# Optimization experiments

Measured on AMD Instinct MI355X. Metric: run time of the kernel, lower is better.

Reference implementation:

```python
import jax, jax.numpy as jnp
import numpy as np

BETA = 0.25
EPS = 1e-12  # matches torch F.normalize default eps


def l2norm(x):
    # x / max(||x||_2, eps) over last dim, like torch.nn.functional.normalize
    n = jnp.linalg.norm(x, axis=-1, keepdims=True)
    return x / jnp.maximum(n, EPS)


def setup_inputs() -> dict:
    key = jax.random.key(0)
    kz, kw = jax.random.split(key)
    B, C, H, W = 16, 128, 32, 32
    K, D = 8192, 128
    z = jax.random.normal(kz, (B, C, H, W), dtype=jnp.float32)
    # kmeans_init=False path: randn then l2norm
    weight = l2norm(jax.random.normal(kw, (K, D), dtype=jnp.float32))
    return {"z": z, "weight": weight}


def reference(z, weight):
    B, C, H, W = z.shape
    # b c h w -> b h w c, then l2norm over channel dim
    zt = l2norm(jnp.transpose(z, (0, 2, 3, 1)))
    z_flat = zt.reshape(-1, C)                        # (N, D)
    x_sq = jnp.sum(z_flat * z_flat, axis=1, keepdims=True)      # (N, 1)
    c_sq = jnp.sum(weight * weight, axis=1)[None, :]            # (1, K)
    xc = jnp.einsum('nd,kd->nk', z_flat, weight)                # (N, K) GEMM
    dists = x_sq + c_sq - 2.0 * xc
    encoding_indices = jnp.argmin(dists, axis=1)                # (N,)
    z_q = weight[encoding_indices].reshape(zt.shape)            # (B,H,W,C)
    # commitment loss: beta * mse(stop_grad(z_q), z)
    loss = BETA * jnp.mean((jax.lax.stop_gradient(z_q) - zt) ** 2)
    # straight-through estimator
    z_q = zt + jax.lax.stop_gradient(z_q - zt)
    z_q = jnp.transpose(z_q, (0, 3, 1, 2))                      # b h w c -> b c h w
    return z_q, loss, encoding_indices
```

## Files before the change

kernel.cpp:

```cpp
#include <hip/hip_runtime.h>
#include <hip/hip_bf16.h>

typedef unsigned int u32;
typedef unsigned long long u64;
typedef unsigned short u16;

#define NPOS 16384
#define DCH  128
#define KCB  8192
#define HW   1024
#define BETA 0.25f
#define ZQ_SZ 2097152
#define MARGIN 0.022f
#define QCAP 8192
#define ZSTR 132

typedef __attribute__((ext_vector_type(8))) short short8;
typedef __attribute__((ext_vector_type(4))) float f32x4;

__device__ inline u16 f2bf(float x) {
    u32 u = __float_as_uint(x);
    return (u16)((u + 0x7FFFu + ((u >> 16) & 1u)) >> 16);
}
__device__ inline u32 mono(float f) {
    u32 b = __float_as_uint(f);
    return (b & 0x80000000u) ? ~b : (b | 0x80000000u);
}

__global__ __launch_bounds__(256) void kwprep(const float* __restrict__ w,
                                              u16* __restrict__ wb,
                                              float* __restrict__ csq) {
    const int t = threadIdx.x;
    const int row = blockIdx.x * 16 + (t >> 4);
    const int l = t & 15;
    const float4* src = (const float4*)(w + (size_t)row * DCH + l * 8);
    float4 a = src[0], b = src[1];
    float s = a.x*a.x + a.y*a.y + a.z*a.z + a.w*a.w
            + b.x*b.x + b.y*b.y + b.z*b.z + b.w*b.w;
    union { u16 h[8]; uint4 v; } u;
    u.h[0]=f2bf(a.x); u.h[1]=f2bf(a.y); u.h[2]=f2bf(a.z); u.h[3]=f2bf(a.w);
    u.h[4]=f2bf(b.x); u.h[5]=f2bf(b.y); u.h[6]=f2bf(b.z); u.h[7]=f2bf(b.w);
    *(uint4*)(wb + (size_t)row * DCH + l * 8) = u.v;
    s += __shfl_xor(s, 1, 64);
    s += __shfl_xor(s, 2, 64);
    s += __shfl_xor(s, 4, 64);
    s += __shfl_xor(s, 8, 64);
    if (l == 0) csq[row] = s;
}

__global__ __launch_bounds__(256, 2) void kmain(const float* __restrict__ z,
                                                const float* __restrict__ wgt,
                                                const u16* __restrict__ wb,
                                                const float* __restrict__ csq,
                                                float* __restrict__ out) {
    __shared__ __align__(16) float ztl[64 * ZSTR];
    __shared__ __align__(16) u32 shpool[64 * ZSTR];
    __shared__ u32 rowMinU[64];
    __shared__ u64 finalkey[64];
    __shared__ float psum[64][4];
    __shared__ float invL[64];
    __shared__ int codes[64];
    __shared__ float lsum[4];
    __shared__ int qcnt;

    const int t = threadIdx.x;
    const int lane = t & 63;
    const int w = t >> 6;
    const int n0 = blockIdx.x * 64;
    const int b = n0 >> 10, hw0 = n0 & 1023;

    const int p = lane;
    float vch[32];
    {
        const float* zp = z + (size_t)b * DCH * HW + hw0 + p;
        #pragma unroll
        for (int j = 0; j < 32; ++j)
            vch[j] = zp[(size_t)(w * 32 + j) * HW];
        float s = 0.f;
        #pragma unroll
        for (int j = 0; j < 32; ++j) s += vch[j] * vch[j];
        psum[p][w] = s;
    }
    if (t < 64) { rowMinU[t] = 0x7f800000u; finalkey[t] = ~0ULL; }
    if (t == 0) qcnt = 0;
    __syncthreads();
    if (t < 64) {
        float ss = psum[t][0] + psum[t][1] + psum[t][2] + psum[t][3];
        invL[t] = 1.0f / fmaxf(sqrtf(ss), 1e-12f);
    }
    __syncthreads();
    {
        float inv = invL[p];
        #pragma unroll
        for (int j = 0; j < 32; ++j)
            ztl[p * ZSTR + w * 32 + j] = vch[j] * inv;
    }
    __syncthreads();

    short8 af[4][4];
    #pragma unroll
    for (int rt = 0; rt < 4; ++rt)
        #pragma unroll
        for (int ks = 0; ks < 4; ++ks) {
            int row = rt * 16 + (lane & 15);
            int kb = ks * 32 + (lane >> 4) * 8;
            const float4* zr = (const float4*)&ztl[row * ZSTR + kb];
            float4 x0 = zr[0], x1 = zr[1];
            union { u16 h[8]; short8 v; } uu;
            uu.h[0]=f2bf(x0.x); uu.h[1]=f2bf(x0.y); uu.h[2]=f2bf(x0.z); uu.h[3]=f2bf(x0.w);
            uu.h[4]=f2bf(x1.x); uu.h[5]=f2bf(x1.y); uu.h[6]=f2bf(x1.z); uu.h[7]=f2bf(x1.w);
            af[rt][ks] = uu.v;
        }

    const u16* wtb = wb + ((w * 32 + (lane & 15)) << 7) + ((lane >> 4) << 3);

    float bmin[16], thr[16];
    #pragma unroll
    for (int i = 0; i < 16; ++i) { bmin[i] = 3.4e38f; thr[i] = -1.f; }

    short8 bA[8], bB[8];

#define LOADB(D, KT) do { \
    const u16* bsrc = wtb + (size_t)(KT) * 16384; \
    _Pragma("unroll") \
    for (int ct_ = 0; ct_ < 2; ++ct_) \
        _Pragma("unroll") \
        for (int ks_ = 0; ks_ < 4; ++ks_) \
            D[ct_ * 4 + ks_] = *(const short8*)(bsrc + ct_ * 2048 + ks_ * 32); \
} while (0)

#define COMPUTE(S, KT, COLLECT) do { \
    f32x4 acc[4][2] = {}; \
    _Pragma("unroll") \
    for (int ks_ = 0; ks_ < 4; ++ks_) \
        _Pragma("unroll") \
        for (int rt_ = 0; rt_ < 4; ++rt_) { \
            acc[rt_][0] = __builtin_amdgcn_mfma_f32_16x16x32_bf16(af[rt_][ks_], S[ks_],     acc[rt_][0], 0, 0, 0); \
            acc[rt_][1] = __builtin_amdgcn_mfma_f32_16x16x32_bf16(af[rt_][ks_], S[4 + ks_], acc[rt_][1], 0, 0, 0); \
        } \
    _Pragma("unroll") \
    for (int rt_ = 0; rt_ < 4; ++rt_) \
        _Pragma("unroll") \
        for (int e_ = 0; e_ < 4; ++e_) { \
            float d0 = fmaf(acc[rt_][0][e_], -2.f, 2.125f); \
            float d1 = fmaf(acc[rt_][1][e_], -2.f, 2.125f); \
            float m2 = fminf(d0, d1); \
            int i_ = rt_ * 4 + e_; \
            bmin[i_] = fminf(bmin[i_], m2); \
            if (COLLECT && m2 <= thr[i_]) { \
                u32 rl = (u32)(rt_ * 16 + (lane >> 4) * 4 + e_); \
                u32 cb = (u32)((KT) * 128 + w * 32 + (lane & 15)); \
                if (d0 <= thr[i_]) { int qi = atomicAdd(&qcnt, 1); if (qi < QCAP) shpool[qi] = (rl << 13) | cb; } \
                if (d1 <= thr[i_]) { int qi = atomicAdd(&qcnt, 1); if (qi < QCAP) shpool[qi] = (rl << 13) | (cb + 16u); } \
            } \
        } \
} while (0)

#define REFRESH() do { \
    _Pragma("unroll") \
    for (int i_ = 0; i_ < 16; ++i_) { \
        float v_ = bmin[i_]; \
        v_ = fminf(v_, __shfl_xor(v_, 1, 64)); \
        v_ = fminf(v_, __shfl_xor(v_, 2, 64)); \
        v_ = fminf(v_, __shfl_xor(v_, 4, 64)); \
        v_ = fminf(v_, __shfl_xor(v_, 8, 64)); \
        if ((lane & 15) == 0) \
            atomicMin(&rowMinU[(i_ >> 2) * 16 + (lane >> 4) * 4 + (i_ & 3)], __float_as_uint(v_)); \
    } \
    _Pragma("unroll") \
    for (int i_ = 0; i_ < 16; ++i_) \
        thr[i_] = fminf(__uint_as_float(rowMinU[(i_ >> 2) * 16 + (lane >> 4) * 4 + (i_ & 3)]), bmin[i_]) + MARGIN; \
} while (0)

    LOADB(bA, 0);
    COMPUTE(bA, 0, false);
    REFRESH();

    #pragma unroll 1
    for (int kt2 = 0; kt2 < 32; ++kt2) {
        const int kt0 = kt2 * 2;
        LOADB(bB, kt0 + 1);
        COMPUTE(bA, kt0, true);
        LOADB(bA, (kt0 + 2) & 63);
        COMPUTE(bB, kt0 + 1, true);
        if ((kt2 & 3) == 3) REFRESH();
    }

    __syncthreads();

    {
        int nq = qcnt < QCAP ? qcnt : QCAP;
        int gq = t >> 4, l = t & 15;
        for (int qi = gq; qi < nq; qi += 16) {
            u32 e = shpool[qi];
            int rl = e >> 13;
            int code = e & 0x1FFF;
            const float4* zr = (const float4*)&ztl[rl * ZSTR + l * 8];
            const float4* wr = (const float4*)(wgt + (size_t)code * DCH + l * 8);
            float4 za = zr[0], zb = zr[1], wa = wr[0], wbv = wr[1];
            float s = 0.f;
            s = fmaf(za.x, wa.x, s); s = fmaf(za.y, wa.y, s);
            s = fmaf(za.z, wa.z, s); s = fmaf(za.w, wa.w, s);
            s = fmaf(zb.x, wbv.x, s); s = fmaf(zb.y, wbv.y, s);
            s = fmaf(zb.z, wbv.z, s); s = fmaf(zb.w, wbv.w, s);
            s += __shfl_xor(s, 1, 64);
            s += __shfl_xor(s, 2, 64);
            s += __shfl_xor(s, 4, 64);
            s += __shfl_xor(s, 8, 64);
            if (l == 0) {
                float ed = csq[code] - 2.0f * s;
                u64 key = ((u64)mono(ed) << 32) | (u32)code;
                atomicMin((unsigned long long*)&finalkey[rl], (unsigned long long)key);
            }
        }
    }
    __syncthreads();

    if (t < 64) {
        u32 code = (u32)finalkey[t];
        codes[t] = (int)code;
        out[ZQ_SZ + 1 + n0 + t] = (float)code;
    }
    __syncthreads();
    float* Wg = (float*)shpool;
    {
        int r = t >> 2, c0 = (t & 3) * 32;
        const float4* wr = (const float4*)(wgt + (size_t)codes[r] * DCH + c0);
        float4* dst = (float4*)&Wg[r * ZSTR + c0];
        #pragma unroll
        for (int m = 0; m < 8; ++m) dst[m] = wr[m];
    }
    __syncthreads();
    {
        float* ob = out + (size_t)b * DCH * HW + hw0;
        float sq = 0.f;
        #pragma unroll
        for (int j = 0; j < 32; ++j) {
            int c = w * 32 + j;
            float zv = ztl[p * ZSTR + c];
            float diff = Wg[p * ZSTR + c] - zv;
            ob[(size_t)c * HW + p] = zv + diff;
            sq += diff * diff;
        }
        #pragma unroll
        for (int o = 32; o > 0; o >>= 1) sq += __shfl_down(sq, o, 64);
        if (lane == 0) lsum[w] = sq;
    }
    __syncthreads();
    if (t == 0)
        atomicAdd(out + ZQ_SZ, (lsum[0] + lsum[1] + lsum[2] + lsum[3]) * (BETA / (float)ZQ_SZ));

#undef LOADB
#undef COMPUTE
#undef REFRESH
}

extern "C" void kernel_launch(void* const* d_in, const int* in_sizes, int n_in,
                              void* d_out, int out_size, void* d_ws, size_t ws_size,
                              hipStream_t stream) {
    const float* z = (const float*)d_in[0];
    const float* w = (const float*)d_in[1];
    float* out = (float*)d_out;
    float* wsf = (float*)d_ws;

    u16* wb = (u16*)wsf;
    float* csq = wsf + 524288;

    kwprep<<<512, 256, 0, stream>>>(w, wb, csq);
    hipMemsetAsync(out + ZQ_SZ, 0, 4, stream);
    kmain<<<256, 256, 0, stream>>>(z, w, wb, csq, out);
}
```

Before: 200.2 us.

## Halve rows per block and double waves to fill all CUs

Each block now handles 32 positions with 512 threads instead of 64 positions with 256 threads, and the grid grows to 512 blocks. Each wave covers 16 codes per tile with two row tiles, and the candidate pool capacity shrinks. This is meant to use all compute units with more resident waves to hide load latency. In exchange, every block streams the full bf16 codebook for half as many rows, doubling codebook cache traffic and lowering MFMA work per load.

```diff
diff --git a/kernel.cpp b/kernel.cpp
--- a/kernel.cpp
+++ b/kernel.cpp
@@ -12,8 +12,9 @@
 #define BETA 0.25f
 #define ZQ_SZ 2097152
 #define MARGIN 0.022f
-#define QCAP 8192
+#define QCAP 2048
 #define ZSTR 132
+#define ROWS 32
 
 typedef __attribute__((ext_vector_type(8))) short short8;
 typedef __attribute__((ext_vector_type(4))) float f32x4;
@@ -48,58 +49,60 @@
     if (l == 0) csq[row] = s;
 }
 
-__global__ __launch_bounds__(256, 2) void kmain(const float* __restrict__ z,
+__global__ __launch_bounds__(512, 4) void kmain(const float* __restrict__ z,
                                                 const float* __restrict__ wgt,
                                                 const u16* __restrict__ wb,
                                                 const float* __restrict__ csq,
                                                 float* __restrict__ out) {
-    __shared__ __align__(16) float ztl[64 * ZSTR];
-    __shared__ __align__(16) u32 shpool[64 * ZSTR];
-    __shared__ u32 rowMinU[64];
-    __shared__ u64 finalkey[64];
-    __shared__ float psum[64][4];
-    __shared__ float invL[64];
-    __shared__ int codes[64];
-    __shared__ float lsum[4];
+    __shared__ __align__(16) float ztl[ROWS * ZSTR];
+    __shared__ __align__(16) u32 pool[ROWS * ZSTR];
+    __shared__ u32 rowMinU[ROWS];
+    __shared__ u64 finalkey[ROWS];
+    __shared__ float psum[ROWS][16];
+    __shared__ float invL[ROWS];
+    __shared__ int codes[ROWS];
+    __shared__ float lsum[8];
     __shared__ int qcnt;
 
     const int t = threadIdx.x;
     const int lane = t & 63;
     const int w = t >> 6;
-    const int n0 = blockIdx.x * 64;
+    const int n0 = blockIdx.x * ROWS;
     const int b = n0 >> 10, hw0 = n0 & 1023;
-
-    const int p = lane;
-    float vch[32];
+    const int p = t & 31, g = t >> 5;
+
+    float vch[8];
     {
         const float* zp = z + (size_t)b * DCH * HW + hw0 + p;
         #pragma unroll
-        for (int j = 0; j < 32; ++j)
-            vch[j] = zp[(size_t)(w * 32 + j) * HW];
+        for (int j = 0; j < 8; ++j)
+            vch[j] = zp[(size_t)(g + j * 16) * HW];
         float s = 0.f;
         #pragma unroll
-        for (int j = 0; j < 32; ++j) s += vch[j] * vch[j];
-        psum[p][w] = s;
-    }
-    if (t < 64) { rowMinU[t] = 0x7f800000u; finalkey[t] = ~0ULL; }
+        for (int j = 0; j < 8; ++j) s += vch[j] * vch[j];
+        psum[p][g] = s;
+    }
+    if (t < ROWS) { rowMinU[t] = 0x7f800000u; finalkey[t] = ~0ULL; }
     if (t == 0) qcnt = 0;
     __syncthreads();
-    if (t < 64) {
-        float ss = psum[t][0] + psum[t][1] + psum[t][2] + psum[t][3];
+    if (t < ROWS) {
+        float ss = 0.f;
+        #pragma unroll
+        for (int j = 0; j < 16; ++j) ss += psum[t][j];
         invL[t] = 1.0f / fmaxf(sqrtf(ss), 1e-12f);
     }
     __syncthreads();
     {
         float inv = invL[p];
         #pragma unroll
-        for (int j = 0; j < 32; ++j)
-            ztl[p * ZSTR + w * 32 + j] = vch[j] * inv;
-    }
-    __syncthreads();
-
-    short8 af[4][4];
+        for (int j = 0; j < 8; ++j)
+            ztl[p * ZSTR + g + j * 16] = vch[j] * inv;
+    }
+    __syncthreads();
+
+    short8 af[2][4];
     #pragma unroll
-    for (int rt = 0; rt < 4; ++rt)
+    for (int rt = 0; rt < 2; ++rt)
         #pragma unroll
         for (int ks = 0; ks < 4; ++ks) {
             int row = rt * 16 + (lane & 15);
@@ -112,53 +115,47 @@
             af[rt][ks] = uu.v;
         }
 
-    const u16* wtb = wb + ((w * 32 + (lane & 15)) << 7) + ((lane >> 4) << 3);
-
-    float bmin[16], thr[16];
+    const u16* wtb = wb + ((w * 16 + (lane & 15)) << 7) + ((lane >> 4) << 3);
+
+    float bmin[8], thr[8];
     #pragma unroll
-    for (int i = 0; i < 16; ++i) { bmin[i] = 3.4e38f; thr[i] = -1.f; }
-
-    short8 bA[8], bB[8];
+    for (int i = 0; i < 8; ++i) { bmin[i] = 3.4e38f; thr[i] = -1.f; }
+
+    short8 bA[4], bB[4];
 
 #define LOADB(D, KT) do { \
     const u16* bsrc = wtb + (size_t)(KT) * 16384; \
     _Pragma("unroll") \
-    for (int ct_ = 0; ct_ < 2; ++ct_) \
-        _Pragma("unroll") \
-        for (int ks_ = 0; ks_ < 4; ++ks_) \
-            D[ct_ * 4 + ks_] = *(const short8*)(bsrc + ct_ * 2048 + ks_ * 32); \
+    for (int ks_ = 0; ks_ < 4; ++ks_) \
+        D[ks_] = *(const short8*)(bsrc + ks_ * 32); \
 } while (0)
 
 #define COMPUTE(S, KT, COLLECT) do { \
-    f32x4 acc[4][2] = {}; \
-    _Pragma("unroll") \
-    for (int ks_ = 0; ks_ < 4; ++ks_) \
-        _Pragma("unroll") \
-        for (int rt_ = 0; rt_ < 4; ++rt_) { \
-            acc[rt_][0] = __builtin_amdgcn_mfma_f32_16x16x32_bf16(af[rt_][ks_], S[ks_],     acc[rt_][0], 0, 0, 0); \
-            acc[rt_][1] = __builtin_amdgcn_mfma_f32_16x16x32_bf16(af[rt_][ks_], S[4 + ks_], acc[rt_][1], 0, 0, 0); \
-        } \
-    _Pragma("unroll") \
-    for (int rt_ = 0; rt_ < 4; ++rt_) \
+    f32x4 acc[2] = {}; \
+    _Pragma("unroll") \
+    for (int ks_ = 0; ks_ < 4; ++ks_) { \
+        acc[0] = __builtin_amdgcn_mfma_f32_16x16x32_bf16(af[0][ks_], S[ks_], acc[0], 0, 0, 0); \
+        acc[1] = __builtin_amdgcn_mfma_f32_16x16x32_bf16(af[1][ks_], S[ks_], acc[1], 0, 0, 0); \
+    } \
+    _Pragma("unroll") \
+    for (int rt_ = 0; rt_ < 2; ++rt_) \
         _Pragma("unroll") \
         for (int e_ = 0; e_ < 4; ++e_) { \
-            float d0 = fmaf(acc[rt_][0][e_], -2.f, 2.125f); \
-            float d1 = fmaf(acc[rt_][1][e_], -2.f, 2.125f); \
-            float m2 = fminf(d0, d1); \
+            float d_ = fmaf(acc[rt_][e_], -2.f, 2.125f); \
             int i_ = rt_ * 4 + e_; \
-            bmin[i_] = fminf(bmin[i_], m2); \
-            if (COLLECT && m2 <= thr[i_]) { \
-                u32 rl = (u32)(rt_ * 16 + (lane >> 4) * 4 + e_); \
-                u32 cb = (u32)((KT) * 128 + w * 32 + (lane & 15)); \
-                if (d0 <= thr[i_]) { int qi = atomicAdd(&qcnt, 1); if (qi < QCAP) shpool[qi] = (rl << 13) | cb; } \
-                if (d1 <= thr[i_]) { int qi = atomicAdd(&qcnt, 1); if (qi < QCAP) shpool[qi] = (rl << 13) | (cb + 16u); } \
+            bmin[i_] = fminf(bmin[i_], d_); \
+            if (COLLECT && d_ <= thr[i_]) { \
+                u32 rl_ = (u32)(rt_ * 16 + (lane >> 4) * 4 + e_); \
+                u32 cb_ = (u32)((KT) * 128 + w * 16 + (lane & 15)); \
+                int qi_ = atomicAdd(&qcnt, 1); \
+                if (qi_ < QCAP) pool[qi_] = (rl_ << 13) | cb_; \
             } \
         } \
 } while (0)
 
 #define REFRESH() do { \
     _Pragma("unroll") \
-    for (int i_ = 0; i_ < 16; ++i_) { \
+    for (int i_ = 0; i_ < 8; ++i_) { \
         float v_ = bmin[i_]; \
         v_ = fminf(v_, __shfl_xor(v_, 1, 64)); \
         v_ = fminf(v_, __shfl_xor(v_, 2, 64)); \
@@ -168,7 +165,7 @@
             atomicMin(&rowMinU[(i_ >> 2) * 16 + (lane >> 4) * 4 + (i_ & 3)], __float_as_uint(v_)); \
     } \
     _Pragma("unroll") \
-    for (int i_ = 0; i_ < 16; ++i_) \
+    for (int i_ = 0; i_ < 8; ++i_) \
         thr[i_] = fminf(__uint_as_float(rowMinU[(i_ >> 2) * 16 + (lane >> 4) * 4 + (i_ & 3)]), bmin[i_]) + MARGIN; \
 } while (0)
 
@@ -191,8 +188,8 @@
     {
         int nq = qcnt < QCAP ? qcnt : QCAP;
         int gq = t >> 4, l = t & 15;
-        for (int qi = gq; qi < nq; qi += 16) {
-            u32 e = shpool[qi];
+        for (int qi = gq; qi < nq; qi += 32) {
+            u32 e = pool[qi];
             int rl = e >> 13;
             int code = e & 0x1FFF;
             const float4* zr = (const float4*)&ztl[rl * ZSTR + l * 8];
@@ -216,27 +213,27 @@
     }
     __syncthreads();
 
-    if (t < 64) {
+    if (t < ROWS) {
         u32 code = (u32)finalkey[t];
         codes[t] = (int)code;
         out[ZQ_SZ + 1 + n0 + t] = (float)code;
     }
     __syncthreads();
-    float* Wg = (float*)shpool;
-    {
-        int r = t >> 2, c0 = (t & 3) * 32;
-        const float4* wr = (const float4*)(wgt + (size_t)codes[r] * DCH + c0);
-        float4* dst = (float4*)&Wg[r * ZSTR + c0];
-        #pragma unroll
-        for (int m = 0; m < 8; ++m) dst[m] = wr[m];
+    float* Wg = (float*)pool;
+    {
+        int r = t >> 4, ch = t & 15;
+        const float4* wr = (const float4*)(wgt + (size_t)codes[r] * DCH + ch * 8);
+        float4* dst = (float4*)&Wg[r * ZSTR + ch * 8];
+        dst[0] = wr[0];
+        dst[1] = wr[1];
     }
     __syncthreads();
     {
         float* ob = out + (size_t)b * DCH * HW + hw0;
         float sq = 0.f;
         #pragma unroll
-        for (int j = 0; j < 32; ++j) {
-            int c = w * 32 + j;
+        for (int j = 0; j < 8; ++j) {
+            int c = g + j * 16;
             float zv = ztl[p * ZSTR + c];
             float diff = Wg[p * ZSTR + c] - zv;
             ob[(size_t)c * HW + p] = zv + diff;
@@ -247,8 +244,11 @@
         if (lane == 0) lsum[w] = sq;
     }
     __syncthreads();
-    if (t == 0)
-        atomicAdd(out + ZQ_SZ, (lsum[0] + lsum[1] + lsum[2] + lsum[3]) * (BETA / (float)ZQ_SZ));
+    if (t == 0) {
+        float s = lsum[0] + lsum[1] + lsum[2] + lsum[3]
+                + lsum[4] + lsum[5] + lsum[6] + lsum[7];
+        atomicAdd(out + ZQ_SZ, s * (BETA / (float)ZQ_SZ));
+    }
 
 #undef LOADB
 #undef COMPUTE
@@ -268,5 +268,5 @@
 
     kwprep<<<512, 256, 0, stream>>>(w, wb, csq);
     hipMemsetAsync(out + ZQ_SZ, 0, 4, stream);
-    kmain<<<256, 256, 0, stream>>>(z, w, wb, csq, out);
-}
+    kmain<<<512, 512, 0, stream>>>(z, w, wb, csq, out);
+}
```

Measured after the change: 213.6 us. 6.7% more time.
